# Optimization experiments

Measured on AMD Instinct MI355X. Metric: run time of the kernel, lower is better.

Reference implementation:

```python
import jax, jax.numpy as jnp
import numpy as np

_PADE_B = np.array([6.476475253248e+16, 3.238237626624e+16, 7771770303897600.0,
                    1187353796428800.0, 129060195264000.0, 10559470521600.0,
                    670442572800.0, 33522128640.0, 1323241920.0, 40840800.0,
                    960960.0, 16380.0, 182.0, 1.0])
_MAXNORM = 5.371920351148152
_MAX_SQUARINGS = 6  # randn 3x3 has Fro norm ~3 < maxnorm; 6 steps is ample headroom


def _expm(A):
    """Batched scaling-and-squaring Pade-13 matrix exponential. A: [N, d, d]."""
    b = _PADE_B.astype(A.dtype)
    d = A.shape[-1]
    ident = jnp.eye(d, dtype=A.dtype)
    fro = jnp.sqrt(jnp.sum(A * A, axis=(1, 2), keepdims=True))  # [N,1,1]
    n_sq = jnp.maximum(0.0, jnp.ceil(jnp.log2(fro / _MAXNORM)))
    Ascaled = A / (2.0 ** n_sq)
    n_sq_i = n_sq.reshape(-1).astype(jnp.int32)  # [N]

    A2 = Ascaled @ Ascaled
    A4 = A2 @ A2
    A6 = A4 @ A2
    U = Ascaled @ (A6 @ (b[13] * A6 + b[11] * A4 + b[9] * A2)
                   + b[7] * A6 + b[5] * A4 + b[3] * A2 + b[1] * ident)
    V = (A6 @ (b[12] * A6 + b[10] * A4 + b[8] * A2)
         + b[6] * A6 + b[4] * A4 + b[2] * A2 + b[0] * ident)
    P = U + V
    Q = -U + V
    R = jnp.linalg.solve(Q, P)  # torch.solve(P, Q): Q X = P

    def body(k, R):
        R2 = R @ R
        return jnp.where((k < n_sq_i)[:, None, None], R2, R)

    return jax.lax.fori_loop(0, _MAX_SQUARINGS, body, R, unroll=True)


def setup_inputs() -> dict:
    key = jax.random.key(0)
    k1, k2, k3 = jax.random.split(key, 3)
    bs, n, d = 65536, 24, 3
    return {
        "mean": jax.random.normal(k1, (bs, n, d), dtype=jnp.float32),
        "var": jax.random.normal(k2, (bs, n, d, d), dtype=jnp.float32),
        "gt": jax.random.normal(k3, (bs, n, d), dtype=jnp.float32),
    }


def reference(mean, var, gt):
    bs, n, d = mean.shape
    A = var.reshape(bs * n, d, d)
    E = _expm(A)                               # [bs*n, d, d]
    delta = (gt - mean).reshape(bs * n, d)     # [bs*n, d]
    quad = jnp.einsum('ni,nij,nj->n', delta, E, delta)
    dets = jnp.linalg.det(A)
    per = 0.5 * (quad + dets) / n              # [bs*n]
    loss = per.reshape(bs, n).sum(axis=1)      # [bs]
    return loss.mean()
```

## Files before the change

### kernel.cpp

```cpp
#include <hip/hip_runtime.h>

#define TPB 256

#define B0c  6.476475253248e+16f
#define B1c  3.238237626624e+16f
#define B2c  7.7717703038976e+15f
#define B3c  1.1873537964288e+15f
#define B4c  1.29060195264e+14f
#define B5c  1.05594705216e+13f
#define B6c  6.704425728e+11f
#define B7c  3.352212864e+10f
#define B8c  1.32324192e+9f
#define B9c  4.08408e+7f
#define B10c 9.6096e+5f
#define B11c 1.638e+4f
#define B12c 182.0f
#define B13c 1.0f

__device__ __forceinline__ float pick4(bool o1, bool o2, float x0, float x1,
                                       float x2, float x3) {
  const float a = o1 ? x1 : x0;
  const float b = o1 ? x3 : x2;
  return o2 ? b : a;
}

__global__ __launch_bounds__(TPB) void expm_loss_kernel(
    const float* __restrict__ mean, const float* __restrict__ var,
    const float* __restrict__ gt, float* __restrict__ partials) {
  const int tid = threadIdx.x;
  const long long i = (long long)blockIdx.x * TPB + tid;

  const long long e9 = i * 9;
  const long long vb = e9 >> 2;
  const int voff = (int)(e9 & 3);
  const float4* v4 = (const float4*)var;
  const float4 w0 = v4[vb], w1 = v4[vb + 1], w2 = v4[vb + 2];

  const long long e3 = i * 3;
  const long long mb = e3 >> 2;
  const int moff = (int)(e3 & 3);
  const long long mlast = ((long long)gridDim.x * TPB * 3 >> 2) - 1;
  const long long mb1 = mb + 1 <= mlast ? mb + 1 : mlast;
  const float4* m4 = (const float4*)mean;
  const float4* g4 = (const float4*)gt;
  const float4 mw0 = m4[mb], mw1 = m4[mb1];
  const float4 gw0 = g4[mb], gw1 = g4[mb1];

  const bool v1b = (voff & 1), v2b = (voff & 2);
  const float a0 = pick4(v1b, v2b, w0.x, w0.y, w0.z, w0.w);
  const float a1 = pick4(v1b, v2b, w0.y, w0.z, w0.w, w1.x);
  const float a2 = pick4(v1b, v2b, w0.z, w0.w, w1.x, w1.y);
  const float a3 = pick4(v1b, v2b, w0.w, w1.x, w1.y, w1.z);
  const float a4 = pick4(v1b, v2b, w1.x, w1.y, w1.z, w1.w);
  const float a5 = pick4(v1b, v2b, w1.y, w1.z, w1.w, w2.x);
  const float a6 = pick4(v1b, v2b, w1.z, w1.w, w2.x, w2.y);
  const float a7 = pick4(v1b, v2b, w1.w, w2.x, w2.y, w2.z);
  const float a8 = pick4(v1b, v2b, w2.x, w2.y, w2.z, w2.w);

  const bool m1b = (moff & 1), m2b = (moff & 2);
  const float me0 = pick4(m1b, m2b, mw0.x, mw0.y, mw0.z, mw0.w);
  const float me1 = pick4(m1b, m2b, mw0.y, mw0.z, mw0.w, mw1.x);
  const float me2 = pick4(m1b, m2b, mw0.z, mw0.w, mw1.x, mw1.y);
  const float ge0 = pick4(m1b, m2b, gw0.x, gw0.y, gw0.z, gw0.w);
  const float ge1 = pick4(m1b, m2b, gw0.y, gw0.z, gw0.w, gw1.x);
  const float ge2 = pick4(m1b, m2b, gw0.z, gw0.w, gw1.x, gw1.y);

  const float d0 = ge0 - me0, d1 = ge1 - me1, d2 = ge2 - me2;

  const float detA = a0 * (a4 * a8 - a5 * a7)
                   - a1 * (a3 * a8 - a5 * a6)
                   + a2 * (a3 * a7 - a4 * a6);
  const float trA = a0 + a4 + a8;
  const float trA2 = fmaf(a0, a0, fmaf(a4, a4, a8 * a8))
                   + 2.0f * (fmaf(a1, a3, fmaf(a2, a6, a5 * a7)));
  float fro2 = fmaf(a0, a0, fmaf(a1, a1, a2 * a2));
  fro2 = fmaf(a3, a3, fmaf(a4, a4, fmaf(a5, a5, fro2)));
  fro2 = fmaf(a6, a6, fmaf(a7, a7, fmaf(a8, a8, fro2)));
  const float u0 = fmaf(a0, d0, fmaf(a1, d1, a2 * d2));
  const float u1 = fmaf(a3, d0, fmaf(a4, d1, a5 * d2));
  const float u2 = fmaf(a6, d0, fmaf(a7, d1, a8 * d2));
  const float v0 = fmaf(a0, d0, fmaf(a3, d1, a6 * d2));
  const float v1 = fmaf(a1, d0, fmaf(a4, d1, a7 * d2));
  const float v2 = fmaf(a2, d0, fmaf(a5, d1, a8 * d2));
  const float dAd  = fmaf(d0, u0, fmaf(d1, u1, d2 * u2));
  const float dA2d = fmaf(v0, u0, fmaf(v1, u1, v2 * u2));
  const float dd   = fmaf(d0, d0, fmaf(d1, d1, d2 * d2));

  const float nsqf = fmaxf(0.0f, ceilf(fmaf(0.5f, __log2f(fro2), -2.4253625f)));
  int nsq = (int)nsqf;
  nsq = nsq > 6 ? 6 : nsq;
  const float scl = exp2f(-nsqf);
  const float scl2 = scl * scl;

  const float t = scl * trA;
  const float trB2 = scl2 * trA2;
  const float m = 0.5f * fmaf(t, t, -trB2);
  const float dch = detA * scl2 * scl;

  const float x4p = fmaf(t, t, -m), x4q = fmaf(-t, m, dch), x4r = t * dch;
  const float x5p = fmaf(x4p, t, x4q), x5q = fmaf(-x4p, m, x4r), x5r = x4p * dch;
  const float x6p = fmaf(x5p, t, x5q), x6q = fmaf(-x5p, m, x5r), x6r = x5p * dch;

  const float w1p = fmaf(B11c, x4p, x6p) + B9c;
  const float w1q = fmaf(B11c, x4q, x6q);
  const float w1r = fmaf(B11c, x4r, x6r);
  const float s4a = x6p * w1p;
  const float s3a = fmaf(x6p, w1q, x6q * w1p);
  const float gp = fmaf(s4a, x4p, fmaf(s3a, t,   fmaf(x6p, w1r, fmaf(x6r, w1p, x6q * w1q))));
  const float gq = fmaf(s4a, x4q, fmaf(-s3a, m,  fmaf(x6q, w1r, x6r * w1q)));
  const float gr = fmaf(s4a, x4r, fmaf(s3a, dch, x6r * w1r));
  const float uep = fmaf(B7c, x6p, fmaf(B5c, x4p, gp)) + B3c;
  const float ueq = fmaf(B7c, x6q, fmaf(B5c, x4q, gq));
  const float uer = fmaf(B7c, x6r, fmaf(B5c, x4r, gr)) + B1c;
  const float up = fmaf(uep, t, ueq);
  const float uq = fmaf(-uep, m, uer);
  const float ur = uep * dch;

  const float w2p = fmaf(B12c, x6p, fmaf(B10c, x4p, B8c));
  const float w2q = fmaf(B12c, x6q, B10c * x4q);
  const float w2r = fmaf(B12c, x6r, B10c * x4r);
  const float s4b = x6p * w2p;
  const float s3b = fmaf(x6p, w2q, x6q * w2p);
  const float hp = fmaf(s4b, x4p, fmaf(s3b, t,   fmaf(x6p, w2r, fmaf(x6r, w2p, x6q * w2q))));
  const float hq = fmaf(s4b, x4q, fmaf(-s3b, m,  fmaf(x6q, w2r, x6r * w2q)));
  const float hr = fmaf(s4b, x4r, fmaf(s3b, dch, x6r * w2r));
  const float vp = fmaf(B6c, x6p, fmaf(B4c, x4p, hp)) + B2c;
  const float vq = fmaf(B6c, x6q, fmaf(B4c, x4q, hq));
  const float vr = fmaf(B6c, x6r, fmaf(B4c, x4r, hr)) + B0c;

  const float s = 1.0f / B0c;
  const float pp = (vp + up) * s, pq = (vq + uq) * s, pr = (vr + ur) * s;
  const float qp = (vp - up) * s, qq = (vq - uq) * s, qr = (vr - ur) * s;

  const float qpp = qp * qp, qpq2 = 2.0f * qp * qq;
  const float a2t = fmaf(qpp, x4p, fmaf(qpq2, t,   fmaf(2.0f * qp, qr, qq * qq)));
  const float b2t = fmaf(qpp, x4q, fmaf(-qpq2, m,  2.0f * qq * qr));
  const float c2t = fmaf(qpp, x4r, fmaf(qpq2, dch, qr * qr));
  const float tQ = fmaf(qp, trB2, fmaf(qq, t, 3.0f * qr));
  const float trQ2 = fmaf(a2t, trB2, fmaf(b2t, t, 3.0f * c2t));
  const float mQ = 0.5f * fmaf(tQ, tQ, -trQ2);
  const float detQ =
      qp * (fmaf(qp, fmaf(qp, dch * dch, fmaf(qq, m * dch, qr * fmaf(m, m, -2.0f * t * dch))),
                 fmaf(qq, fmaf(qq, t * dch, qr * fmaf(t, m, -3.0f * dch)),
                      qr * qr * fmaf(t, t, -2.0f * m))))
    + qq * fmaf(qq, fmaf(qq, dch, qr * m), qr * qr * t)
    + qr * qr * qr;
  float inv = __builtin_amdgcn_rcpf(detQ);
  inv = inv * (2.0f - detQ * inv);
  const float jp = fmaf(-tQ, qp, a2t);
  const float jq = fmaf(-tQ, qq, b2t);
  const float jr = fmaf(-tQ, qr, c2t) + mQ;

  const float s4 = pp * jp;
  const float s3 = fmaf(pp, jq, pq * jp);
  float rp = fmaf(s4, x4p, fmaf(s3, t,   fmaf(pp, jr, fmaf(pr, jp, pq * jq)))) * inv;
  float rq = fmaf(s4, x4q, fmaf(-s3, m,  fmaf(pq, jr, pr * jq))) * inv;
  float rr = fmaf(s4, x4r, fmaf(s3, dch, pr * jr)) * inv;

  for (int k = 0; k < nsq; ++k) {
    const float rp2 = rp * rp, rpq2 = 2.0f * rp * rq;
    const float nrp = fmaf(rp2, x4p, fmaf(rpq2, t,   fmaf(2.0f * rp, rr, rq * rq)));
    const float nrq = fmaf(rp2, x4q, fmaf(-rpq2, m,  2.0f * rq * rr));
    const float nrr = fmaf(rp2, x4r, fmaf(rpq2, dch, rr * rr));
    rp = nrp; rq = nrq; rr = nrr;
  }

  const float quad = fmaf(rp, scl2 * dA2d, fmaf(rq, scl * dAd, rr * dd));
  float val = 0.5f * (quad + detA);

#pragma unroll
  for (int offx = 32; offx > 0; offx >>= 1) val += __shfl_down(val, offx, 64);
  __shared__ float wsum[TPB / 64];
  if ((tid & 63) == 0) wsum[tid >> 6] = val;
  __syncthreads();
  if (tid == 0) {
    float b = 0.f;
#pragma unroll
    for (int wi = 0; wi < TPB / 64; ++wi) b += wsum[wi];
    partials[blockIdx.x] = b;
  }
}

#define RTPB 1024
__global__ __launch_bounds__(RTPB) void reduce_partials_kernel(
    const float* __restrict__ partials, int n, double inv_total,
    float* __restrict__ out) {
  double s = 0.0;
  for (int i = threadIdx.x; i < n; i += RTPB) s += (double)partials[i];
#pragma unroll
  for (int off = 32; off > 0; off >>= 1) s += __shfl_down(s, off, 64);
  __shared__ double ds[RTPB / 64];
  if ((threadIdx.x & 63) == 0) ds[threadIdx.x >> 6] = s;
  __syncthreads();
  if (threadIdx.x == 0) {
    double b = 0.0;
#pragma unroll
    for (int w = 0; w < RTPB / 64; ++w) b += ds[w];
    out[0] = (float)(b * inv_total);
  }
}

extern "C" void kernel_launch(void* const* d_in, const int* in_sizes, int n_in,
                              void* d_out, int out_size, void* d_ws, size_t ws_size,
                              hipStream_t stream) {
  const float* mean = (const float*)d_in[0];
  const float* var  = (const float*)d_in[1];
  const float* gt   = (const float*)d_in[2];
  const int nmat    = in_sizes[1] / 9;
  const int nblocks = nmat / TPB;
  float* partials   = (float*)d_ws;

  expm_loss_kernel<<<nblocks, TPB, 0, stream>>>(mean, var, gt, partials);
  reduce_partials_kernel<<<1, RTPB, 0, stream>>>(partials, nblocks,
                                                 1.0 / (double)nmat,
                                                 (float*)d_out);
}
```

Baseline: 25.00 us.

## Process four matrices per thread with aligned float4 loads, drop the realignment selects

Each thread now handles four consecutive 3x3 matrices, so their 36 floats and 12 mean/gt floats align exactly to float4 boundaries. That lets every load be a plain aligned vector load with no per-element offset selection or overlapping loads. The grid shrinks by a factor of four, which cuts partial sums and the final reduce to 256 threads. In exchange each thread uses more registers and loads are strided per lane, which may hurt coalescing and occupancy.

```diff
diff --git a/kernel.cpp b/kernel.cpp
--- a/kernel.cpp
+++ b/kernel.cpp
@@ -17,56 +17,9 @@
 #define B12c 182.0f
 #define B13c 1.0f
 
-__device__ __forceinline__ float pick4(bool o1, bool o2, float x0, float x1,
-                                       float x2, float x3) {
-  const float a = o1 ? x1 : x0;
-  const float b = o1 ? x3 : x2;
-  return o2 ? b : a;
-}
-
-__global__ __launch_bounds__(TPB) void expm_loss_kernel(
-    const float* __restrict__ mean, const float* __restrict__ var,
-    const float* __restrict__ gt, float* __restrict__ partials) {
-  const int tid = threadIdx.x;
-  const long long i = (long long)blockIdx.x * TPB + tid;
-
-  const long long e9 = i * 9;
-  const long long vb = e9 >> 2;
-  const int voff = (int)(e9 & 3);
-  const float4* v4 = (const float4*)var;
-  const float4 w0 = v4[vb], w1 = v4[vb + 1], w2 = v4[vb + 2];
-
-  const long long e3 = i * 3;
-  const long long mb = e3 >> 2;
-  const int moff = (int)(e3 & 3);
-  const long long mlast = ((long long)gridDim.x * TPB * 3 >> 2) - 1;
-  const long long mb1 = mb + 1 <= mlast ? mb + 1 : mlast;
-  const float4* m4 = (const float4*)mean;
-  const float4* g4 = (const float4*)gt;
-  const float4 mw0 = m4[mb], mw1 = m4[mb1];
-  const float4 gw0 = g4[mb], gw1 = g4[mb1];
-
-  const bool v1b = (voff & 1), v2b = (voff & 2);
-  const float a0 = pick4(v1b, v2b, w0.x, w0.y, w0.z, w0.w);
-  const float a1 = pick4(v1b, v2b, w0.y, w0.z, w0.w, w1.x);
-  const float a2 = pick4(v1b, v2b, w0.z, w0.w, w1.x, w1.y);
-  const float a3 = pick4(v1b, v2b, w0.w, w1.x, w1.y, w1.z);
-  const float a4 = pick4(v1b, v2b, w1.x, w1.y, w1.z, w1.w);
-  const float a5 = pick4(v1b, v2b, w1.y, w1.z, w1.w, w2.x);
-  const float a6 = pick4(v1b, v2b, w1.z, w1.w, w2.x, w2.y);
-  const float a7 = pick4(v1b, v2b, w1.w, w2.x, w2.y, w2.z);
-  const float a8 = pick4(v1b, v2b, w2.x, w2.y, w2.z, w2.w);
-
-  const bool m1b = (moff & 1), m2b = (moff & 2);
-  const float me0 = pick4(m1b, m2b, mw0.x, mw0.y, mw0.z, mw0.w);
-  const float me1 = pick4(m1b, m2b, mw0.y, mw0.z, mw0.w, mw1.x);
-  const float me2 = pick4(m1b, m2b, mw0.z, mw0.w, mw1.x, mw1.y);
-  const float ge0 = pick4(m1b, m2b, gw0.x, gw0.y, gw0.z, gw0.w);
-  const float ge1 = pick4(m1b, m2b, gw0.y, gw0.z, gw0.w, gw1.x);
-  const float ge2 = pick4(m1b, m2b, gw0.z, gw0.w, gw1.x, gw1.y);
-
-  const float d0 = ge0 - me0, d1 = ge1 - me1, d2 = ge2 - me2;
-
+__device__ __forceinline__ float expm_loss_one(
+    float a0, float a1, float a2, float a3, float a4, float a5,
+    float a6, float a7, float a8, float d0, float d1, float d2) {
   const float detA = a0 * (a4 * a8 - a5 * a7)
                    - a1 * (a3 * a8 - a5 * a6)
                    + a2 * (a3 * a7 - a4 * a6);
@@ -166,7 +119,31 @@
   }
 
   const float quad = fmaf(rp, scl2 * dA2d, fmaf(rq, scl * dAd, rr * dd));
-  float val = 0.5f * (quad + detA);
+  return 0.5f * (quad + detA);
+}
+
+__global__ __launch_bounds__(TPB) void expm_loss_kernel(
+    const float* __restrict__ mean, const float* __restrict__ var,
+    const float* __restrict__ gt, float* __restrict__ partials) {
+  const int tid = threadIdx.x;
+  const long long ti = (long long)blockIdx.x * TPB + tid;
+
+  const float4* vp = (const float4*)var + ti * 9;
+  const float4 w0 = vp[0], w1 = vp[1], w2 = vp[2], w3 = vp[3], w4 = vp[4],
+               w5 = vp[5], w6 = vp[6], w7 = vp[7], w8 = vp[8];
+  const float4* mp = (const float4*)mean + ti * 3;
+  const float4* gp = (const float4*)gt + ti * 3;
+  const float4 mw0 = mp[0], mw1 = mp[1], mw2 = mp[2];
+  const float4 gw0 = gp[0], gw1 = gp[1], gw2 = gp[2];
+
+  float val = expm_loss_one(w0.x, w0.y, w0.z, w0.w, w1.x, w1.y, w1.z, w1.w, w2.x,
+                            gw0.x - mw0.x, gw0.y - mw0.y, gw0.z - mw0.z);
+  val += expm_loss_one(w2.y, w2.z, w2.w, w3.x, w3.y, w3.z, w3.w, w4.x, w4.y,
+                       gw0.w - mw0.w, gw1.x - mw1.x, gw1.y - mw1.y);
+  val += expm_loss_one(w4.z, w4.w, w5.x, w5.y, w5.z, w5.w, w6.x, w6.y, w6.z,
+                       gw1.z - mw1.z, gw1.w - mw1.w, gw2.x - mw2.x);
+  val += expm_loss_one(w6.w, w7.x, w7.y, w7.z, w7.w, w8.x, w8.y, w8.z, w8.w,
+                       gw2.y - mw2.y, gw2.z - mw2.z, gw2.w - mw2.w);
 
 #pragma unroll
   for (int offx = 32; offx > 0; offx >>= 1) val += __shfl_down(val, offx, 64);
@@ -181,23 +158,18 @@
   }
 }
 
-#define RTPB 1024
-__global__ __launch_bounds__(RTPB) void reduce_partials_kernel(
+__global__ __launch_bounds__(256) void reduce_partials_kernel(
     const float* __restrict__ partials, int n, double inv_total,
     float* __restrict__ out) {
   double s = 0.0;
-  for (int i = threadIdx.x; i < n; i += RTPB) s += (double)partials[i];
+  for (int i = threadIdx.x; i < n; i += 256) s += (double)partials[i];
 #pragma unroll
   for (int off = 32; off > 0; off >>= 1) s += __shfl_down(s, off, 64);
-  __shared__ double ds[RTPB / 64];
+  __shared__ double ds[4];
   if ((threadIdx.x & 63) == 0) ds[threadIdx.x >> 6] = s;
   __syncthreads();
-  if (threadIdx.x == 0) {
-    double b = 0.0;
-#pragma unroll
-    for (int w = 0; w < RTPB / 64; ++w) b += ds[w];
-    out[0] = (float)(b * inv_total);
-  }
+  if (threadIdx.x == 0)
+    out[0] = (float)((ds[0] + ds[1] + ds[2] + ds[3]) * inv_total);
 }
 
 extern "C" void kernel_launch(void* const* d_in, const int* in_sizes, int n_in,
@@ -207,11 +179,11 @@
   const float* var  = (const float*)d_in[1];
   const float* gt   = (const float*)d_in[2];
   const int nmat    = in_sizes[1] / 9;
-  const int nblocks = nmat / TPB;
+  const int nblocks = nmat / (TPB * 4);
   float* partials   = (float*)d_ws;
 
   expm_loss_kernel<<<nblocks, TPB, 0, stream>>>(mean, var, gt, partials);
-  reduce_partials_kernel<<<1, RTPB, 0, stream>>>(partials, nblocks,
-                                                 1.0 / (double)nmat,
-                                                 (float*)d_out);
+  reduce_partials_kernel<<<1, 256, 0, stream>>>(partials, nblocks,
+                                                1.0 / (double)nmat,
+                                                (float*)d_out);
 }
```

Measured after the change: 23.81 us, median of 2. 1.05x faster.
